# Kernel optimization log

Measured on AMD Instinct MI355X. Metric: run time of the kernel, lower is better.

## Reference

```python
import jax, jax.numpy as jnp
import numpy as np

E = 2048        # embed_dim
H = 16          # num_heads
D = 128         # head_dim
K = 4           # num_hyper_nodes (timelines)
N = 4096        # seq_len
B = 1           # batch (module asserts batch==1)
CAP_FACTOR = 1.25
CAP = int(N / K * CAP_FACTOR)   # 1280, static
ROPE_BASE = 10000.0
SCALE = D ** -0.5
NEG_INF = jnp.float32(-1e30)


def setup_inputs() -> dict:
    key = jax.random.key(0)
    ks = jax.random.split(key, 10)
    def xavier(k, shape):
        fan_in, fan_out = shape[0], shape[1]
        lim = np.sqrt(6.0 / (fan_in + fan_out))
        return jax.random.uniform(k, shape, jnp.float32, -lim, lim)
    return {
        'x':   jax.random.normal(ks[0], (B, N, E), jnp.float32),
        # weights stored (in, out); equivalent to torch Linear weight.T
        'Wq':  xavier(ks[1], (E, H * D)),
        'Wk':  xavier(ks[2], (E, H * D)),
        'Wv':  xavier(ks[3], (E, H * D)),
        'Wo':  xavier(ks[4], (H * D, E)),
        'Wr1': xavier(ks[5], (E, E // 2)),
        'br1': jnp.zeros((E // 2,), jnp.float32),
        'Wr2': xavier(ks[6], (E // 2, K)),
        'br2': jnp.zeros((K,), jnp.float32),
    }


def _rope_tables():
    # local positions: arange(CAP) (use_local_rope=True)
    inv_freq = 1.0 / (ROPE_BASE ** (jnp.arange(0, D, 2, dtype=jnp.float32) / D))
    freqs = jnp.arange(CAP, dtype=jnp.float32)[:, None] * inv_freq[None, :]  # (CAP, D/2)
    emb = jnp.concatenate([freqs, freqs], axis=-1)  # (CAP, D)
    return jnp.cos(emb), jnp.sin(emb)


def _rotate_half(t):
    return jnp.concatenate([-t[..., D // 2:], t[..., :D // 2]], axis=-1)


def reference(x, Wq, Wk, Wv, Wo, Wr1, br1, Wr2, br2):
    # --- expert-choice routing ---
    h = jax.nn.gelu(x @ Wr1 + br1, approximate=False)      # (B, N, E/2)
    scores = h @ Wr2 + br2                                  # (B, N, K)
    scores_t = scores[0].T                                  # (K, N)
    topk_scores, topk_idx = jax.lax.top_k(scores_t, CAP)    # (K, CAP)
    sel_w = jax.nn.softmax(topk_scores, axis=-1)            # (K, CAP)
    aux_loss = -jnp.mean(jnp.max(scores, axis=-1))

    # --- projections ---
    q = (x @ Wq).reshape(B, N, H, D).transpose(0, 2, 1, 3)  # (B, H, N, D)
    k = (x @ Wk).reshape(B, N, H, D).transpose(0, 2, 1, 3)
    v = (x @ Wv).reshape(B, N, H, D).transpose(0, 2, 1, 3)

    cos, sin = _rope_tables()                               # (CAP, D)
    causal = jnp.tril(jnp.ones((CAP, CAP), bool))

    def timeline(idx, w):
        # gather this timeline's tokens
        qt = q[:, :, idx]                                   # (B, H, CAP, D)
        kt = k[:, :, idx]
        vt = v[:, :, idx]
        qt = qt * cos + _rotate_half(qt) * sin
        kt = kt * cos + _rotate_half(kt) * sin
        att = jnp.einsum('bhqd,bhkd->bhqk', qt, kt) * SCALE
        att = jnp.where(causal, att, NEG_INF)
        att = jax.nn.softmax(att, axis=-1)
        o = jnp.einsum('bhqk,bhkd->bhqd', att, vt)          # (B, H, CAP, D)
        return o * w[None, None, :, None]                   # weighted combine

    outs = jax.vmap(timeline)(topk_idx, sel_w)              # (K, B, H, CAP, D)

    # scatter back: sum contributions over timelines
    idx_flat = topk_idx.reshape(-1)                         # (K*CAP,)
    vals = outs.transpose(1, 2, 0, 3, 4).reshape(B, H, K * CAP, D)
    out = jnp.zeros((B, H, N, D), x.dtype).at[:, :, idx_flat, :].add(vals)

    out = out.transpose(0, 2, 1, 3).reshape(B, N, H * D) @ Wo  # (B, N, E)
    return out, aux_loss
```

## Files before the change

### kernel.cpp

```cpp
#include <hip/hip_runtime.h>
#include <cstdint>
#include <cstddef>

#define N_TOK 4096
#define E_DIM 2048
#define NH    16
#define DH    128
#define KEXP  4
#define CAPN  1280
#define NTILE 20
#define NQB   10
#define QKV_STRIDE 6144
#define SCALE_QK 0.08838834764831845f
#define LOG2E    1.4426950408889634f
#define NEG_BIG -1e30f

typedef __attribute__((ext_vector_type(4))) float f32x4;
typedef __attribute__((ext_vector_type(8))) short s16x8;

__device__ __forceinline__ float bf2f(unsigned short u){
  union{unsigned int i; float fl;} c; c.i = ((unsigned int)u)<<16; return c.fl;
}
__device__ __forceinline__ unsigned short f2bf(float x){
  union{float fl; unsigned int i;} c; c.fl=x;
  return (unsigned short)((c.i + 0x7FFFu + ((c.i>>16)&1u))>>16);
}
__device__ __forceinline__ f32x4 mfma_bf16(s16x8 a, s16x8 b, f32x4 c){
  asm("v_mfma_f32_16x16x32_bf16 %0, %1, %2, %0" : "+v"(c) : "v"(a), "v"(b));
  return c;
}
__device__ __forceinline__ void gl_lds16(const unsigned short* g, unsigned short* l){
  __builtin_amdgcn_global_load_lds(
      (const __attribute__((address_space(1))) unsigned int*)g,
      (__attribute__((address_space(3))) unsigned int*)l, 16, 0, 0);
}

__global__ __launch_bounds__(256) void conv_x_kernel(const float* __restrict__ x,
    unsigned short* __restrict__ hi, unsigned short* __restrict__ lo, int n4){
  int idx = blockIdx.x*256 + threadIdx.x;
  if (idx >= n4) return;
  float4 v = ((const float4*)x)[idx];
  float ar[4] = {v.x, v.y, v.z, v.w};
  union{ unsigned short u[4]; uint2 q; } H, L;
  #pragma unroll
  for(int i=0;i<4;i++){
    unsigned short h = f2bf(ar[i]);
    H.u[i] = h;
    L.u[i] = f2bf(ar[i] - bf2f(h));
  }
  ((uint2*)hi)[idx] = H.q;
  ((uint2*)lo)[idx] = L.q;
}

__global__ __launch_bounds__(256) void tconv_kernel(const float* __restrict__ W,
    unsigned short* __restrict__ Thi, unsigned short* __restrict__ Tlo, int R, int C){
  __shared__ float t[32][33];
  int tx = threadIdx.x, ty = threadIdx.y;
  int c0 = blockIdx.x*32, r0 = blockIdx.y*32;
  #pragma unroll
  for(int i=0;i<4;i++){
    int r = r0 + ty + i*8;
    t[ty+i*8][tx] = W[(size_t)r*C + c0 + tx];
  }
  __syncthreads();
  #pragma unroll
  for(int i=0;i<4;i++){
    int c = c0 + ty + i*8;
    float v = t[tx][ty+i*8];
    size_t o = (size_t)c*R + r0 + tx;
    unsigned short h = f2bf(v);
    Thi[o] = h;
    if (Tlo) Tlo[o] = f2bf(v - bf2f(h));
  }
}

__global__ __launch_bounds__(256) void tconv4_kernel(const float* __restrict__ W0,
    const float* __restrict__ W1, const float* __restrict__ W2, const float* __restrict__ W3,
    unsigned short* __restrict__ out){
  __shared__ float t[32][33];
  int z = blockIdx.z;
  const float* W = (z==0)?W0 : (z==1)?W1 : (z==2)?W2 : W3;
  unsigned short* T = out + (size_t)z*E_DIM*E_DIM;
  int tx = threadIdx.x, ty = threadIdx.y;
  int c0 = blockIdx.x*32, r0 = blockIdx.y*32;
  #pragma unroll
  for(int i=0;i<4;i++){
    int r = r0 + ty + i*8;
    t[ty+i*8][tx] = W[(size_t)r*E_DIM + c0 + tx];
  }
  __syncthreads();
  #pragma unroll
  for(int i=0;i<4;i++){
    int c = c0 + ty + i*8;
    T[(size_t)c*E_DIM + r0 + tx] = f2bf(t[tx][ty+i*8]);
  }
}

template<int OUTBF>
__global__ __launch_bounds__(512, 2) void gemm_p(
    const unsigned short* __restrict__ A, const unsigned short* __restrict__ Bt,
    void* __restrict__ Cp, int N, int Kd){
  __shared__ __align__(16) unsigned short lds[3*12288];
  const int tid = threadIdx.x;
  const int w = tid>>6, lane = tid&63, g = lane>>4, r16 = lane&15;
  const int wm = w>>2, wn = w&3;
  const int mb = blockIdx.y, nb = blockIdx.x;
  const unsigned short* Ab = A  + (size_t)mb*128*Kd;
  const unsigned short* Bb = Bt + (size_t)nb*256*Kd;
  const int PMAX = Kd >> 5;

  f32x4 acc[4][4];
  #pragma unroll
  for(int i=0;i<4;i++)
    #pragma unroll
    for(int j=0;j<4;j++) acc[i][j] = f32x4{0.f,0.f,0.f,0.f};

  auto stageP = [&](int Pst, int slot){
    unsigned short* base = &lds[slot*12288];
    const int col = Pst*32;
    {
      int row = tid>>2, ch = tid&3;
      int sc = ch ^ ((row>>1)&3);
      gl_lds16(Ab + (size_t)row*Kd + col + sc*8, base + tid*8);
    }
    #pragma unroll
    for(int i=0;i<2;i++){
      int n = i*512 + tid;
      int rw = n>>2, c2 = n&3;
      int s2 = c2 ^ ((rw>>1)&3);
      gl_lds16(Bb + (size_t)rw*Kd + col + s2*8, base + 4096 + n*8);
    }
  };
  const int xoff = (g ^ ((r16>>1)&3)) << 3;

  stageP(0,0); stageP(1,1);
  asm volatile("s_waitcnt vmcnt(3)" ::: "memory");
  __builtin_amdgcn_s_barrier();

  int sR = 0, sW = 2;
  for(int P=0; P<PMAX; ++P){
    const unsigned short* base = &lds[sR*12288];
    s16x8 af[4], bfv[4];
    #pragma unroll
    for(int mf=0;mf<4;mf++)
      af[mf] = *(const s16x8*)&base[(wm*64 + mf*16 + r16)*32 + xoff];
    #pragma unroll
    for(int nf=0;nf<4;nf++)
      bfv[nf] = *(const s16x8*)&base[4096 + (wn*64 + nf*16 + r16)*32 + xoff];
    if (P+2 < PMAX) stageP(P+2, sW);
    __builtin_amdgcn_s_setprio(1);
    #pragma unroll
    for(int mf=0;mf<4;mf++)
      #pragma unroll
      for(int nf=0;nf<4;nf++)
        acc[mf][nf] = mfma_bf16(af[mf], bfv[nf], acc[mf][nf]);
    __builtin_amdgcn_s_setprio(0);
    if      (P+2 < PMAX) asm volatile("s_waitcnt vmcnt(3)" ::: "memory");
    else                 asm volatile("s_waitcnt vmcnt(0)" ::: "memory");
    __builtin_amdgcn_s_barrier();
    sR = (sR==2) ? 0 : sR+1;
    sW = (sW==2) ? 0 : sW+1;
  }

  const int rowb = mb*128 + wm*64, colb = nb*256 + wn*64;
  #pragma unroll
  for(int mf=0;mf<4;mf++)
    #pragma unroll
    for(int nf=0;nf<4;nf++)
      #pragma unroll
      for(int r=0;r<4;r++){
        int rr = rowb + mf*16 + 4*g + r;
        int cc = colb + nf*16 + r16;
        size_t o = (size_t)rr*N + cc;
        if (OUTBF) ((unsigned short*)Cp)[o] = f2bf(acc[mf][nf][r]);
        else       ((float*)Cp)[o] = acc[mf][nf][r];
      }
}

__global__ __launch_bounds__(512, 1) void gemm_router_p(
    const unsigned short* __restrict__ Ahi, const unsigned short* __restrict__ Alo,
    const unsigned short* __restrict__ Bhi, const unsigned short* __restrict__ Blo,
    const float* __restrict__ br1, float* __restrict__ H){
  __shared__ __align__(16) unsigned short lds[2][32768];
  const int tid = threadIdx.x;
  const int w = tid>>6, lane = tid&63, g = lane>>4, r16 = lane&15;
  const int wm = w>>2, wn = w&3;
  const int mb = blockIdx.y, nb = blockIdx.x;
  const unsigned short* AbH = Ahi + (size_t)mb*128*E_DIM;
  const unsigned short* AbL = Alo + (size_t)mb*128*E_DIM;
  const unsigned short* BbH = Bhi + (size_t)nb*128*E_DIM;
  const unsigned short* BbL = Blo + (size_t)nb*128*E_DIM;
  const int NT = E_DIM >> 6;

  f32x4 acc[4][2];
  #pragma unroll
  for(int i=0;i<4;i++){ acc[i][0]=f32x4{0.f,0.f,0.f,0.f}; acc[i][1]=f32x4{0.f,0.f,0.f,0.f}; }

  auto stage = [&](int buf, int ks, int t){
    int row = tid>>2, ch = tid&3;
    int sc = ch ^ ((row>>1)&3);
    size_t go = (size_t)row*E_DIM + t*64 + ks*32 + sc*8;
    unsigned short* base = &lds[buf][ks*16384];
    gl_lds16(AbH + go, base +         tid*8);
    gl_lds16(AbL + go, base +  4096 + tid*8);
    gl_lds16(BbH + go, base +  8192 + tid*8);
    gl_lds16(BbL + go, base + 12288 + tid*8);
  };
  const int xoff = (g ^ ((r16>>1)&3)) << 3;

  stage(0,0,0); stage(0,1,0); stage(1,0,1);
  asm volatile("s_waitcnt vmcnt(8)" ::: "memory");
  __builtin_amdgcn_s_barrier();

  int cur = 0;
  for(int t=0; t<NT; ++t){
    const int nxt = cur^1;
    #pragma unroll
    for(int ph=0; ph<2; ph++){
      const unsigned short* base = &lds[cur][ph*16384];
      s16x8 ah[4], al[4], bh[2], bl[2];
      #pragma unroll
      for(int mf=0;mf<4;mf++){
        int ro = (wm*64 + mf*16 + r16)*32 + xoff;
        ah[mf] = *(const s16x8*)&base[ro];
        al[mf] = *(const s16x8*)&base[4096 + ro];
      }
      #pragma unroll
      for(int nf=0;nf<2;nf++){
        int ro = (wn*32 + nf*16 + r16)*32 + xoff;
        bh[nf] = *(const s16x8*)&base[8192 + ro];
        bl[nf] = *(const s16x8*)&base[12288 + ro];
      }
      if (ph==0){
        if (t+1 < NT){ stage(nxt,1,t+1); asm volatile("s_waitcnt vmcnt(8)" ::: "memory"); }
        else         {                   asm volatile("s_waitcnt vmcnt(0)" ::: "memory"); }
      } else {
        if (t+2 < NT){ stage(cur,0,t+2); asm volatile("s_waitcnt vmcnt(8)" ::: "memory"); }
        else if (t+1 < NT){              asm volatile("s_waitcnt vmcnt(4)" ::: "memory"); }
        else              {              asm volatile("s_waitcnt vmcnt(0)" ::: "memory"); }
      }
      __builtin_amdgcn_s_barrier();
      __builtin_amdgcn_s_setprio(1);
      #pragma unroll
      for(int mf=0;mf<4;mf++)
        #pragma unroll
        for(int nf=0;nf<2;nf++){
          acc[mf][nf] = mfma_bf16(ah[mf], bh[nf], acc[mf][nf]);
          acc[mf][nf] = mfma_bf16(ah[mf], bl[nf], acc[mf][nf]);
          acc[mf][nf] = mfma_bf16(al[mf], bh[nf], acc[mf][nf]);
        }
      __builtin_amdgcn_s_setprio(0);
      __builtin_amdgcn_s_barrier();
    }
    cur ^= 1;
  }

  const int rowb = mb*128 + wm*64, colb = nb*128 + wn*32;
  #pragma unroll
  for(int mf=0;mf<4;mf++)
    #pragma unroll
    for(int nf=0;nf<2;nf++)
      #pragma unroll
      for(int r=0;r<4;r++){
        int rr = rowb + mf*16 + 4*g + r;
        int cc = colb + nf*16 + r16;
        float v = acc[mf][nf][r] + br1[cc];
        H[(size_t)rr*1024 + cc] = 0.5f*v*(1.0f + erff(v*0.70710678118654752f));
      }
}

__global__ __launch_bounds__(256) void scores_kernel(const float* __restrict__ h,
    const float* __restrict__ Wr2, const float* __restrict__ br2,
    float* __restrict__ scores, float* __restrict__ tokmax){
  int tid = threadIdx.x;
  int n = blockIdx.x*4 + (tid>>6);
  int lane = tid & 63;
  const float* hr = h + (size_t)n*1024;
  float s0=0,s1=0,s2=0,s3=0;
  #pragma unroll
  for(int i=0;i<16;i++){
    int j = lane + i*64;
    float hv = hr[j];
    float4 wv = *(const float4*)(Wr2 + (size_t)j*4);
    s0 += hv*wv.x; s1 += hv*wv.y; s2 += hv*wv.z; s3 += hv*wv.w;
  }
  #pragma unroll
  for(int m=32;m>=1;m>>=1){
    s0 += __shfl_xor(s0,m); s1 += __shfl_xor(s1,m);
    s2 += __shfl_xor(s2,m); s3 += __shfl_xor(s3,m);
  }
  if (lane==0){
    s0+=br2[0]; s1+=br2[1]; s2+=br2[2]; s3+=br2[3];
    scores[n*4+0]=s0; scores[n*4+1]=s1; scores[n*4+2]=s2; scores[n*4+3]=s3;
    tokmax[n]=fmaxf(fmaxf(s0,s1),fmaxf(s2,s3));
  }
}

__global__ __launch_bounds__(1024) void aux_kernel(const float* __restrict__ tokmax, float* __restrict__ out_aux){
  __shared__ float red[1024];
  int t = threadIdx.x;
  red[t] = tokmax[t] + tokmax[t+1024] + tokmax[t+2048] + tokmax[t+3072];
  __syncthreads();
  for(int k=512;k>=1;k>>=1){ if(t<k) red[t]+=red[t+k]; __syncthreads(); }
  if (t==0) out_aux[0] = -red[0]/4096.0f;
}

__global__ __launch_bounds__(256) void rank_kernel(const float* __restrict__ scores,
    int* __restrict__ topk_idx, float* __restrict__ topv, int* __restrict__ rank_of){
  __shared__ unsigned long long keys[4096];
  const int e = blockIdx.y, blk = blockIdx.x, tid = threadIdx.x;
  for(int i=tid;i<4096;i+=256){
    unsigned u = __float_as_uint(scores[i*4+e]);
    unsigned m = (u & 0x80000000u) ? ~u : (u | 0x80000000u);
    keys[i] = (((unsigned long long)m)<<32) | (unsigned)(4095-i);
  }
  __syncthreads();
  const int i = blk*256 + tid;
  const unsigned long long mykey = keys[i];
  int cnt = 0;
  #pragma unroll 8
  for(int j=0;j<4096;j++) cnt += (keys[j] > mykey) ? 1 : 0;
  if (cnt < CAPN){
    topk_idx[e*CAPN + cnt] = i;
    topv[e*CAPN + cnt]     = scores[i*4+e];
    rank_of[e*4096 + i]    = cnt;
  } else {
    rank_of[e*4096 + i]    = -1;
  }
}

__global__ __launch_bounds__(1024) void selw_kernel(const float* __restrict__ topv,
    float* __restrict__ sel_w){
  __shared__ float red[1024];
  const int e = blockIdx.x, t = threadIdx.x;
  const float mx = topv[e*CAPN];
  float p0 = expf(topv[e*CAPN + t] - mx);
  float p1 = (t + 1024 < CAPN) ? expf(topv[e*CAPN + t + 1024] - mx) : 0.f;
  red[t] = p0 + p1;
  __syncthreads();
  for(int k=512;k>=1;k>>=1){ if(t<k) red[t]+=red[t+k]; __syncthreads(); }
  const float denom = red[0];
  sel_w[e*CAPN + t] = p0/denom;
  if (t + 1024 < CAPN) sel_w[e*CAPN + t + 1024] = p1/denom;
}

__global__ __launch_bounds__(256) void rope_kernel(float* __restrict__ cosT, float* __restrict__ sinT){
  int idx = blockIdx.x*256 + threadIdx.x;
  int p = idx>>6, dm = idx&63;
  float inv = powf(10000.0f, -(float)dm/64.0f);
  float ang = (float)p*inv;
  cosT[idx]=cosf(ang);
  sinT[idx]=sinf(ang);
}

__global__ __launch_bounds__(256) void prerope_k_kernel(const unsigned short* __restrict__ kb,
    const int* __restrict__ topk_idx, const float* __restrict__ cosT, const float* __restrict__ sinT,
    unsigned short* __restrict__ Kg){
  int idx = blockIdx.x*256 + threadIdx.x;
  int ch = idx & 15;
  int rest = idx >> 4;
  int rank = rest % CAPN;
  int he = rest / CAPN;
  int e = he >> 4, h = he & 15;
  int tok = topk_idx[e*CAPN + rank];
  int d0 = ch*8;
  const unsigned short* krow = kb + (size_t)tok*QKV_STRIDE + h*DH;
  unsigned short held[8], part[8];
  *(uint4*)held = *(const uint4*)(krow + d0);
  *(uint4*)part = *(const uint4*)(krow + (d0^64));
  const float* cr = cosT + rank*64;
  const float* sr = sinT + rank*64;
  float sgn = (d0<64) ? -1.f : 1.f;
  unsigned short outv[8];
  #pragma unroll
  for(int jj=0;jj<8;jj++){
    int dm = (d0+jj)&63;
    outv[jj] = f2bf(bf2f(held[jj])*cr[dm] + sgn*bf2f(part[jj])*sr[dm]);
  }
  int t = rank >> 6, row = rank & 63;
  size_t tbase = ((size_t)(he)*NTILE + t) * 8192;
  *(uint4*)(Kg + tbase + row*128 + ((ch ^ (row&7))<<3)) = *(uint4*)outv;
}

__global__ __launch_bounds__(256) void prev_kernel(const unsigned short* __restrict__ vb,
    const int* __restrict__ topk_idx, unsigned short* __restrict__ Vg){
  __shared__ __align__(16) unsigned short T2[128][72];
  int bid = blockIdx.x;
  int t = bid % NTILE, h = (bid/NTILE) & 15, e = bid/(NTILE*NH);
  int tid = threadIdx.x, lane = tid & 63, dchb = tid >> 6;
  int tok = topk_idx[e*CAPN + t*64 + lane];
  const unsigned short* vrow = vb + (size_t)tok*QKV_STRIDE + h*DH;
  #pragma unroll
  for(int i=0;i<4;i++){
    int d0 = (dchb + i*4)*8;
    unsigned short vv[8];
    *(uint4*)vv = *(const uint4*)(vrow + d0);
    #pragma unroll
    for(int j=0;j<8;j++) T2[d0+j][lane] = vv[j];
  }
  __syncthreads();
  unsigned short* out = Vg + ((size_t)(e*NH+h)*NTILE + t)*8192;
  #pragma unroll
  for(int i=0;i<4;i++){
    int c = i*256 + tid;
    int d = c>>3, ch = c&7;
    *(uint4*)(out + d*64 + ((ch ^ (d&7))<<3)) = *(const uint4*)&T2[d][ch*8];
  }
}

__global__ __launch_bounds__(512) void attn_kernel(
    const unsigned short* __restrict__ qb,
    const unsigned short* __restrict__ Kg, const unsigned short* __restrict__ Vg,
    const int* __restrict__ topk_idx, const float* __restrict__ sel_w,
    const float* __restrict__ cosT, const float* __restrict__ sinT,
    unsigned short* __restrict__ oexp){
  __shared__ __align__(16) unsigned short KsA[2][8192];
  __shared__ __align__(16) unsigned short Vs[8192];
  __shared__ __align__(16) unsigned short Ps[8][16][72];
  const int id = blockIdx.x;
  const int xcd = id & 7, s_ = id >> 3;
  const int qb2 = NQB - 1 - (s_ % NQB);
  const int grp = (s_ / NQB)*8 + xcd;
  const int e = grp >> 4, hh = grp & 15;
  const int tid = threadIdx.x, w = tid>>6, lane = tid&63, g = lane>>4, r16 = lane&15;
  const int* idxE = topk_idx + e*CAPN;
  const unsigned short* Kgb = Kg + (size_t)(e*NH+hh)*CAPN*DH;
  const unsigned short* Vgb = Vg + (size_t)(e*NH+hh)*CAPN*DH;
  const int ktmax = 2*qb2 + 1;

  s16x8 aq[4];
  {
    int qr = qb2*128 + w*16 + r16;
    int tok = idxE[qr];
    const unsigned short* qrow = qb + (size_t)tok*QKV_STRIDE + hh*DH;
    const float* cr = cosT + qr*64;
    const float* sr = sinT + qr*64;
    #pragma unroll
    for(int s=0;s<4;s++){
      int d0 = s*32 + 8*g;
      unsigned short held[8], part[8];
      *(uint4*)held = *(const uint4*)(qrow + d0);
      *(uint4*)part = *(const uint4*)(qrow + (d0^64));
      float sgn = (d0<64) ? -1.f : 1.f;
      union{ s16x8 v; unsigned short u[8]; } fr;
      #pragma unroll
      for(int jj=0;jj<8;jj++){
        int dm = (d0+jj)&63;
        float val = bf2f(held[jj])*cr[dm] + sgn*bf2f(part[jj])*sr[dm];
        fr.u[jj] = f2bf(val * (SCALE_QK*LOG2E));
      }
      aq[s] = fr.v;
    }
  }
  float m_r[4], l_r[4];
  f32x4 o[8];
  #pragma unroll
  for(int r=0;r<4;r++){ m_r[r]=-INFINITY; l_r[r]=0.f; }
  #pragma unroll
  for(int f2=0;f2<8;f2++) o[f2]=f32x4{0.f,0.f,0.f,0.f};

  #pragma unroll
  for(int i=0;i<2;i++){ int c=i*512+tid; gl_lds16(Kgb + c*8, &KsA[0][c*8]); }
  #pragma unroll
  for(int i=0;i<2;i++){ int c=i*512+tid; gl_lds16(Vgb + c*8, &Vs[c*8]); }
  asm volatile("s_waitcnt vmcnt(2)" ::: "memory");
  __builtin_amdgcn_s_barrier();

  for(int kt=0; kt<=ktmax; kt++){
    const int cur = kt & 1;
    if (kt < ktmax){
      const unsigned short* Ksrc = Kgb + (size_t)(kt+1)*8192;
      #pragma unroll
      for(int i=0;i<2;i++){ int c=i*512+tid; gl_lds16(Ksrc + c*8, &KsA[cur^1][c*8]); }
    }
    f32x4 sfr[4];
    #pragma unroll
    for(int fc=0;fc<4;fc++){
      f32x4 a4 = f32x4{0.f,0.f,0.f,0.f};
      const int row = fc*16 + r16;
      #pragma unroll
      for(int s=0;s<4;s++){
        s16x8 bk = *(const s16x8*)&KsA[cur][row*128 + (((s*4+g) ^ (r16&7))<<3)];
        a4 = mfma_bf16(aq[s], bk, a4);
      }
      sfr[fc] = a4;
    }
    if (kt >= 2*qb2){
      #pragma unroll
      for(int fc=0;fc<4;fc++)
        #pragma unroll
        for(int r=0;r<4;r++){
          int qrank  = qb2*128 + w*16 + 4*g + r;
          int kvrank = kt*64 + fc*16 + r16;
          if (kvrank > qrank) sfr[fc][r] = NEG_BIG;
        }
    }
    float corr[4];
    bool need = false;
    #pragma unroll
    for(int r=0;r<4;r++){
      float mx = fmaxf(fmaxf(sfr[0][r],sfr[1][r]), fmaxf(sfr[2][r],sfr[3][r]));
      #pragma unroll
      for(int mk=1;mk<16;mk<<=1) mx = fmaxf(mx, __shfl_xor(mx,mk));
      float nm = fmaxf(m_r[r], mx);
      need = need || (nm > m_r[r]);
      corr[r] = exp2f(m_r[r]-nm);
      m_r[r] = nm;
    }
    if (__any(need)){
      #pragma unroll
      for(int f2=0;f2<8;f2++)
        #pragma unroll
        for(int r=0;r<4;r++) o[f2][r] *= corr[r];
      #pragma unroll
      for(int r=0;r<4;r++) l_r[r] *= corr[r];
    }
    float rs[4] = {0.f,0.f,0.f,0.f};
    #pragma unroll
    for(int fc=0;fc<4;fc++)
      #pragma unroll
      for(int r=0;r<4;r++){
        float p = exp2f(sfr[fc][r] - m_r[r]);
        rs[r] += p;
        Ps[w][4*g+r][fc*16+r16] = f2bf(p);
      }
    #pragma unroll
    for(int r=0;r<4;r++){
      float ts = rs[r];
      #pragma unroll
      for(int mk=1;mk<16;mk<<=1) ts += __shfl_xor(ts,mk);
      l_r[r] += ts;
    }
    if (kt < ktmax) asm volatile("s_waitcnt vmcnt(2)" ::: "memory");
    else            asm volatile("s_waitcnt vmcnt(0)" ::: "memory");
    __builtin_amdgcn_s_barrier();
    #pragma unroll
    for(int ks=0;ks<2;ks++){
      s16x8 pa = *(const s16x8*)&Ps[w][r16][ks*32 + 8*g];
      #pragma unroll
      for(int fd=0;fd<8;fd++){
        const int row = fd*16 + r16;
        s16x8 vf = *(const s16x8*)&Vs[row*64 + (((ks*4+g) ^ (r16&7))<<3)];
        o[fd] = mfma_bf16(pa, vf, o[fd]);
      }
    }
    __builtin_amdgcn_s_barrier();
    if (kt < ktmax){
      const unsigned short* Vsrc = Vgb + (size_t)(kt+1)*8192;
      #pragma unroll
      for(int i=0;i<2;i++){ int c=i*512+tid; gl_lds16(Vsrc + c*8, &Vs[c*8]); }
      asm volatile("s_waitcnt vmcnt(2)" ::: "memory");
      __builtin_amdgcn_s_barrier();
    }
  }
  #pragma unroll
  for(int r=0;r<4;r++){
    int qrank = qb2*128 + w*16 + 4*g + r;
    float fac = sel_w[e*CAPN + qrank] / l_r[r];
    #pragma unroll
    for(int fd=0;fd<8;fd++){
      oexp[((size_t)(e*CAPN + qrank))*E_DIM + hh*DH + fd*16 + r16] = f2bf(o[fd][r]*fac);
    }
  }
}

__global__ __launch_bounds__(256) void acc_kernel(const unsigned short* __restrict__ oexp,
    const int* __restrict__ rank_of, unsigned short* __restrict__ accb){
  int n = blockIdx.x, t = threadIdx.x;
  int base = t*8;
  float s[8] = {0,0,0,0,0,0,0,0};
  #pragma unroll
  for(int e=0;e<4;e++){
    int r = rank_of[e*4096+n];
    if (r>=0){
      union{uint4 q; unsigned short u[8];} ld;
      ld.q = *(const uint4*)(oexp + ((size_t)(e*CAPN+r))*E_DIM + base);
      #pragma unroll
      for(int j2=0;j2<8;j2++) s[j2] += bf2f(ld.u[j2]);
    }
  }
  union{uint4 q; unsigned short u[8];} st;
  #pragma unroll
  for(int j2=0;j2<8;j2++) st.u[j2] = f2bf(s[j2]);
  *(uint4*)(accb + (size_t)n*E_DIM + base) = st.q;
}

extern "C" void kernel_launch(void* const* d_in, const int* in_sizes, int n_in,
                              void* d_out, int out_size, void* d_ws, size_t ws_size,
                              hipStream_t stream) {
  const float* x   = (const float*)d_in[0];
  const float* Wq  = (const float*)d_in[1];
  const float* Wk  = (const float*)d_in[2];
  const float* Wv  = (const float*)d_in[3];
  const float* Wo  = (const float*)d_in[4];
  const float* Wr1 = (const float*)d_in[5];
  const float* br1 = (const float*)d_in[6];
  const float* Wr2 = (const float*)d_in[7];
  const float* br2 = (const float*)d_in[8];

  char* ws = (char*)d_ws;
  size_t off = 0;
  auto alloc = [&](size_t bytes)->void*{
    void* p = ws + off;
    off += (bytes + 255) & ~(size_t)255;
    return p;
  };
  unsigned short* xhi   = (unsigned short*)alloc((size_t)N_TOK*E_DIM*2);
  unsigned short* xlo   = (unsigned short*)alloc((size_t)N_TOK*E_DIM*2);
  unsigned short* wr1hi = (unsigned short*)alloc((size_t)E_DIM*1024*2);
  unsigned short* wr1lo = (unsigned short*)alloc((size_t)E_DIM*1024*2);
  unsigned short* wqkvT = (unsigned short*)alloc((size_t)3*E_DIM*E_DIM*2);
  unsigned short* woT   = (unsigned short*)alloc((size_t)E_DIM*E_DIM*2);
  void* hv = alloc((size_t)KEXP*NH*CAPN*DH*2);
  float* hbuf = (float*)hv;
  unsigned short* Vg = (unsigned short*)hv;
  float* scores = (float*)alloc((size_t)N_TOK*4*4);
  float* tokmax = (float*)alloc((size_t)N_TOK*4);
  int*   topkI  = (int*)alloc((size_t)KEXP*CAPN*4);
  float* topv   = (float*)alloc((size_t)KEXP*CAPN*4);
  float* selw   = (float*)alloc((size_t)KEXP*CAPN*4);
  int*   rankof = (int*)alloc((size_t)KEXP*N_TOK*4);
  float* cosT   = (float*)alloc((size_t)CAPN*64*4);
  float* sinT   = (float*)alloc((size_t)CAPN*64*4);
  unsigned short* qkvbuf = (unsigned short*)alloc((size_t)N_TOK*QKV_STRIDE*2);
  unsigned short* oexp = (unsigned short*)alloc((size_t)KEXP*CAPN*E_DIM*2);
  unsigned short* accb = (unsigned short*)alloc((size_t)N_TOK*E_DIM*2);
  if (off > ws_size) return;

  unsigned short* Kg = xlo;

  conv_x_kernel<<<(N_TOK*E_DIM/4+255)/256, 256, 0, stream>>>(x, xhi, xlo, N_TOK*E_DIM/4);
  tconv_kernel<<<dim3(1024/32, E_DIM/32), dim3(32,8), 0, stream>>>(Wr1, wr1hi, wr1lo, E_DIM, 1024);
  tconv4_kernel<<<dim3(E_DIM/32, E_DIM/32, 4), dim3(32,8), 0, stream>>>(Wq, Wk, Wv, Wo, wqkvT);

  gemm_router_p<<<dim3(8, 32), 512, 0, stream>>>(xhi, xlo, wr1hi, wr1lo, br1, hbuf);
  scores_kernel<<<N_TOK/4, 256, 0, stream>>>(hbuf, Wr2, br2, scores, tokmax);
  aux_kernel<<<1, 1024, 0, stream>>>(tokmax, ((float*)d_out) + (size_t)N_TOK*E_DIM);
  rank_kernel<<<dim3(16, KEXP), 256, 0, stream>>>(scores, topkI, topv, rankof);
  selw_kernel<<<KEXP, 1024, 0, stream>>>(topv, selw);
  rope_kernel<<<CAPN*64/256, 256, 0, stream>>>(cosT, sinT);

  gemm_p<1><<<dim3(QKV_STRIDE/256, N_TOK/128), 512, 0, stream>>>(xhi, wqkvT, qkvbuf, QKV_STRIDE, E_DIM);

  prerope_k_kernel<<<KEXP*NH*CAPN*16/256, 256, 0, stream>>>(qkvbuf + E_DIM, topkI, cosT, sinT, Kg);
  prev_kernel<<<KEXP*NH*NTILE, 256, 0, stream>>>(qkvbuf + 2*E_DIM, topkI, Vg);

  attn_kernel<<<KEXP*NH*NQB, 512, 0, stream>>>(qkvbuf, Kg, Vg, topkI, selw, cosT, sinT, oexp);

  acc_kernel<<<N_TOK, 256, 0, stream>>>(oexp, rankof, accb);

  gemm_p<0><<<dim3(E_DIM/256, N_TOK/128), 512, 0, stream>>>(accb, woT, (float*)d_out, E_DIM, E_DIM);
}
```

Baseline: 430.0 us.

## Load V fragments directly to registers, add lazy softmax rescale and MFMA priority

```diff
diff --git a/kernel.cpp b/kernel.cpp
--- a/kernel.cpp
+++ b/kernel.cpp
@@ -415,7 +415,6 @@
     const float* __restrict__ cosT, const float* __restrict__ sinT,
     unsigned short* __restrict__ oexp){
   __shared__ __align__(16) unsigned short KsA[2][8192];
-  __shared__ __align__(16) unsigned short Vs[8192];
   __shared__ __align__(16) unsigned short Ps[8][16][72];
   const int id = blockIdx.x;
   const int xcd = id & 7, s_ = id >> 3;
@@ -427,6 +426,7 @@
   const unsigned short* Kgb = Kg + (size_t)(e*NH+hh)*CAPN*DH;
   const unsigned short* Vgb = Vg + (size_t)(e*NH+hh)*CAPN*DH;
   const int ktmax = 2*qb2 + 1;
+  const float THR = 8.0f*LOG2E;
 
   s16x8 aq[4];
   {
@@ -461,19 +461,27 @@
 
   #pragma unroll
   for(int i=0;i<2;i++){ int c=i*512+tid; gl_lds16(Kgb + c*8, &KsA[0][c*8]); }
-  #pragma unroll
-  for(int i=0;i<2;i++){ int c=i*512+tid; gl_lds16(Vgb + c*8, &Vs[c*8]); }
-  asm volatile("s_waitcnt vmcnt(2)" ::: "memory");
+  asm volatile("s_waitcnt vmcnt(0)" ::: "memory");
   __builtin_amdgcn_s_barrier();
 
   for(int kt=0; kt<=ktmax; kt++){
     const int cur = kt & 1;
+    const unsigned short* Vt = Vgb + (size_t)kt*8192;
+    s16x8 vfr[2][8];
+    #pragma unroll
+    for(int ks=0;ks<2;ks++){
+      const int sc = ((ks*4+g) ^ (r16&7)) << 3;
+      #pragma unroll
+      for(int fd=0;fd<8;fd++)
+        vfr[ks][fd] = *(const s16x8*)(Vt + (fd*16 + r16)*64 + sc);
+    }
     if (kt < ktmax){
       const unsigned short* Ksrc = Kgb + (size_t)(kt+1)*8192;
       #pragma unroll
       for(int i=0;i<2;i++){ int c=i*512+tid; gl_lds16(Ksrc + c*8, &KsA[cur^1][c*8]); }
     }
     f32x4 sfr[4];
+    __builtin_amdgcn_s_setprio(1);
     #pragma unroll
     for(int fc=0;fc<4;fc++){
       f32x4 a4 = f32x4{0.f,0.f,0.f,0.f};
@@ -485,6 +493,7 @@
       }
       sfr[fc] = a4;
     }
+    __builtin_amdgcn_s_setprio(0);
     if (kt >= 2*qb2){
       #pragma unroll
       for(int fc=0;fc<4;fc++)
@@ -502,8 +511,9 @@
       float mx = fmaxf(fmaxf(sfr[0][r],sfr[1][r]), fmaxf(sfr[2][r],sfr[3][r]));
       #pragma unroll
       for(int mk=1;mk<16;mk<<=1) mx = fmaxf(mx, __shfl_xor(mx,mk));
-      float nm = fmaxf(m_r[r], mx);
-      need = need || (nm > m_r[r]);
+      bool trig = mx > m_r[r] + THR;
+      float nm = trig ? fmaxf(m_r[r], mx) : m_r[r];
+      need = need || trig;
       corr[r] = exp2f(m_r[r]-nm);
       m_r[r] = nm;
     }
@@ -531,25 +541,17 @@
       for(int mk=1;mk<16;mk<<=1) ts += __shfl_xor(ts,mk);
       l_r[r] += ts;
     }
-    if (kt < ktmax) asm volatile("s_waitcnt vmcnt(2)" ::: "memory");
-    else            asm volatile("s_waitcnt vmcnt(0)" ::: "memory");
-    __builtin_amdgcn_s_barrier();
+    __builtin_amdgcn_s_setprio(1);
     #pragma unroll
     for(int ks=0;ks<2;ks++){
       s16x8 pa = *(const s16x8*)&Ps[w][r16][ks*32 + 8*g];
       #pragma unroll
-      for(int fd=0;fd<8;fd++){
-        const int row = fd*16 + r16;
-        s16x8 vf = *(const s16x8*)&Vs[row*64 + (((ks*4+g) ^ (r16&7))<<3)];
-        o[fd] = mfma_bf16(pa, vf, o[fd]);
-      }
-    }
-    __builtin_amdgcn_s_barrier();
+      for(int fd=0;fd<8;fd++)
+        o[fd] = mfma_bf16(pa, vfr[ks][fd], o[fd]);
+    }
+    __builtin_amdgcn_s_setprio(0);
     if (kt < ktmax){
-      const unsigned short* Vsrc = Vgb + (size_t)(kt+1)*8192;
-      #pragma unroll
-      for(int i=0;i<2;i++){ int c=i*512+tid; gl_lds16(Vsrc + c*8, &Vs[c*8]); }
-      asm volatile("s_waitcnt vmcnt(2)" ::: "memory");
+      asm volatile("s_waitcnt vmcnt(0)" ::: "memory");
       __builtin_amdgcn_s_barrier();
     }
   }
```

Result: slower. 471.5 us (+9.6%).

## Retile router GEMM to 64x128 blocks with triple-buffered single-barrier pipeline

Applied to the files above, without the earlier changes.

```diff
diff --git a/kernel.cpp b/kernel.cpp
--- a/kernel.cpp
+++ b/kernel.cpp
@@ -177,85 +177,85 @@
       }
 }
 
-__global__ __launch_bounds__(512, 1) void gemm_router_p(
+__global__ __launch_bounds__(256, 2) void gemm_router_p(
     const unsigned short* __restrict__ Ahi, const unsigned short* __restrict__ Alo,
     const unsigned short* __restrict__ Bhi, const unsigned short* __restrict__ Blo,
     const float* __restrict__ br1, float* __restrict__ H){
-  __shared__ __align__(16) unsigned short lds[2][32768];
+  __shared__ __align__(16) unsigned short lds[3*12288];
   const int tid = threadIdx.x;
   const int w = tid>>6, lane = tid&63, g = lane>>4, r16 = lane&15;
-  const int wm = w>>2, wn = w&3;
   const int mb = blockIdx.y, nb = blockIdx.x;
-  const unsigned short* AbH = Ahi + (size_t)mb*128*E_DIM;
-  const unsigned short* AbL = Alo + (size_t)mb*128*E_DIM;
+  const unsigned short* AbH = Ahi + (size_t)mb*64*E_DIM;
+  const unsigned short* AbL = Alo + (size_t)mb*64*E_DIM;
   const unsigned short* BbH = Bhi + (size_t)nb*128*E_DIM;
   const unsigned short* BbL = Blo + (size_t)nb*128*E_DIM;
-  const int NT = E_DIM >> 6;
+  const int PMAX = E_DIM >> 5;
 
   f32x4 acc[4][2];
   #pragma unroll
   for(int i=0;i<4;i++){ acc[i][0]=f32x4{0.f,0.f,0.f,0.f}; acc[i][1]=f32x4{0.f,0.f,0.f,0.f}; }
 
-  auto stage = [&](int buf, int ks, int t){
-    int row = tid>>2, ch = tid&3;
-    int sc = ch ^ ((row>>1)&3);
-    size_t go = (size_t)row*E_DIM + t*64 + ks*32 + sc*8;
-    unsigned short* base = &lds[buf][ks*16384];
-    gl_lds16(AbH + go, base +         tid*8);
-    gl_lds16(AbL + go, base +  4096 + tid*8);
-    gl_lds16(BbH + go, base +  8192 + tid*8);
-    gl_lds16(BbL + go, base + 12288 + tid*8);
+  auto stageP = [&](int Pst, int slot){
+    unsigned short* base = &lds[slot*12288];
+    const int col = Pst*32;
+    {
+      int row = tid>>2, ch = tid&3;
+      int sc = ch ^ ((row>>1)&3);
+      size_t go = (size_t)row*E_DIM + col + sc*8;
+      gl_lds16(AbH + go, base +        tid*8);
+      gl_lds16(AbL + go, base + 2048 + tid*8);
+    }
+    #pragma unroll
+    for(int i=0;i<2;i++){
+      int n = i*256 + tid;
+      int row = n>>2, ch = n&3;
+      int sc = ch ^ ((row>>1)&3);
+      size_t go = (size_t)row*E_DIM + col + sc*8;
+      gl_lds16(BbH + go, base + 4096 + n*8);
+      gl_lds16(BbL + go, base + 8192 + n*8);
+    }
   };
   const int xoff = (g ^ ((r16>>1)&3)) << 3;
 
-  stage(0,0,0); stage(0,1,0); stage(1,0,1);
-  asm volatile("s_waitcnt vmcnt(8)" ::: "memory");
+  stageP(0,0); stageP(1,1);
+  asm volatile("s_waitcnt vmcnt(6)" ::: "memory");
   __builtin_amdgcn_s_barrier();
 
-  int cur = 0;
-  for(int t=0; t<NT; ++t){
-    const int nxt = cur^1;
-    #pragma unroll
-    for(int ph=0; ph<2; ph++){
-      const unsigned short* base = &lds[cur][ph*16384];
-      s16x8 ah[4], al[4], bh[2], bl[2];
-      #pragma unroll
-      for(int mf=0;mf<4;mf++){
-        int ro = (wm*64 + mf*16 + r16)*32 + xoff;
-        ah[mf] = *(const s16x8*)&base[ro];
-        al[mf] = *(const s16x8*)&base[4096 + ro];
+  int sR = 0, sW = 2;
+  for(int P=0; P<PMAX; ++P){
+    const unsigned short* base = &lds[sR*12288];
+    s16x8 ah[4], al[4], bh[2], bl[2];
+    #pragma unroll
+    for(int mf=0;mf<4;mf++){
+      int ro = (mf*16 + r16)*32 + xoff;
+      ah[mf] = *(const s16x8*)&base[ro];
+      al[mf] = *(const s16x8*)&base[2048 + ro];
+    }
+    #pragma unroll
+    for(int nf=0;nf<2;nf++){
+      int rb = (w*32 + nf*16 + r16)*32 + xoff;
+      bh[nf] = *(const s16x8*)&base[4096 + rb];
+      bl[nf] = *(const s16x8*)&base[8192 + rb];
+    }
+    if (P+2 < PMAX) stageP(P+2, sW);
+    __builtin_amdgcn_s_setprio(1);
+    #pragma unroll
+    for(int mf=0;mf<4;mf++)
+      #pragma unroll
+      for(int nf=0;nf<2;nf++){
+        acc[mf][nf] = mfma_bf16(ah[mf], bh[nf], acc[mf][nf]);
+        acc[mf][nf] = mfma_bf16(ah[mf], bl[nf], acc[mf][nf]);
+        acc[mf][nf] = mfma_bf16(al[mf], bh[nf], acc[mf][nf]);
       }
-      #pragma unroll
-      for(int nf=0;nf<2;nf++){
-        int ro = (wn*32 + nf*16 + r16)*32 + xoff;
-        bh[nf] = *(const s16x8*)&base[8192 + ro];
-        bl[nf] = *(const s16x8*)&base[12288 + ro];
-      }
-      if (ph==0){
-        if (t+1 < NT){ stage(nxt,1,t+1); asm volatile("s_waitcnt vmcnt(8)" ::: "memory"); }
-        else         {                   asm volatile("s_waitcnt vmcnt(0)" ::: "memory"); }
-      } else {
-        if (t+2 < NT){ stage(cur,0,t+2); asm volatile("s_waitcnt vmcnt(8)" ::: "memory"); }
-        else if (t+1 < NT){              asm volatile("s_waitcnt vmcnt(4)" ::: "memory"); }
-        else              {              asm volatile("s_waitcnt vmcnt(0)" ::: "memory"); }
-      }
-      __builtin_amdgcn_s_barrier();
-      __builtin_amdgcn_s_setprio(1);
-      #pragma unroll
-      for(int mf=0;mf<4;mf++)
-        #pragma unroll
-        for(int nf=0;nf<2;nf++){
-          acc[mf][nf] = mfma_bf16(ah[mf], bh[nf], acc[mf][nf]);
-          acc[mf][nf] = mfma_bf16(ah[mf], bl[nf], acc[mf][nf]);
-          acc[mf][nf] = mfma_bf16(al[mf], bh[nf], acc[mf][nf]);
-        }
-      __builtin_amdgcn_s_setprio(0);
-      __builtin_amdgcn_s_barrier();
-    }
-    cur ^= 1;
-  }
-
-  const int rowb = mb*128 + wm*64, colb = nb*128 + wn*32;
+    __builtin_amdgcn_s_setprio(0);
+    if      (P+2 < PMAX) asm volatile("s_waitcnt vmcnt(6)" ::: "memory");
+    else                 asm volatile("s_waitcnt vmcnt(0)" ::: "memory");
+    __builtin_amdgcn_s_barrier();
+    sR = (sR==2) ? 0 : sR+1;
+    sW = (sW==2) ? 0 : sW+1;
+  }
+
+  const int rowb = mb*64, colb = nb*128 + w*32;
   #pragma unroll
   for(int mf=0;mf<4;mf++)
     #pragma unroll
@@ -633,7 +633,7 @@
   tconv_kernel<<<dim3(1024/32, E_DIM/32), dim3(32,8), 0, stream>>>(Wr1, wr1hi, wr1lo, E_DIM, 1024);
   tconv4_kernel<<<dim3(E_DIM/32, E_DIM/32, 4), dim3(32,8), 0, stream>>>(Wq, Wk, Wv, Wo, wqkvT);
 
-  gemm_router_p<<<dim3(8, 32), 512, 0, stream>>>(xhi, xlo, wr1hi, wr1lo, br1, hbuf);
+  gemm_router_p<<<dim3(1024/128, N_TOK/64), 256, 0, stream>>>(xhi, xlo, wr1hi, wr1lo, br1, hbuf);
   scores_kernel<<<N_TOK/4, 256, 0, stream>>>(hbuf, Wr2, br2, scores, tokmax);
   aux_kernel<<<1, 1024, 0, stream>>>(tokmax, ((float*)d_out) + (size_t)N_TOK*E_DIM);
   rank_kernel<<<dim3(16, KEXP), 256, 0, stream>>>(scores, topkI, topv, rankof);
```

Measured after the change: 439.6 us. +2.2%, slower.
